# Kernel tuning notes

Measured on AMD Instinct MI355X. Metric: run time of the kernel, lower is better.

The kernel has to match this reference:

```python
import jax, jax.numpy as jnp
import numpy as np
import math

SIZE = 64
NLAND = 8
N_ITER = 6


def setup_inputs() -> dict:
    key = jax.random.key(0)
    k1, k2, k3 = jax.random.split(key, 3)
    B, T, C = 4, 4096, 1024
    return {
        "q": jax.random.normal(k1, (B, T, C), dtype=jnp.float32),
        "k": jax.random.normal(k2, (B, T, C), dtype=jnp.float32),
        "v": jax.random.normal(k3, (B, T, C), dtype=jnp.float32),
    }


def _iterative_pinv(mat, n_iter=N_ITER):
    # Newton-Schulz iteration for pseudo-inverse of [..., m, m] kernel.
    m = mat.shape[-1]
    I = jnp.eye(m, dtype=mat.dtype)
    K = mat
    # NOTE: torch.max over the whole tensor (global scalar), faithful to source.
    V = (1.0 / jnp.max(jnp.sum(K, axis=-2))) * jnp.swapaxes(K, -1, -2)
    for _ in range(n_iter):
        KV = jnp.matmul(K, V)
        V = jnp.matmul(0.25 * V, 13.0 * I - jnp.matmul(KV, 15.0 * I - jnp.matmul(KV, 7.0 * I - KV)))
    return V


def reference(q, k, v):
    B, T, C = q.shape
    H = C // SIZE
    scale = 1.0 / math.sqrt(SIZE)
    # Faithful reshape (not transpose) as in the source module.
    qh = q.reshape(B, H, T, SIZE)
    kh = k.reshape(B, H, T, SIZE)
    vh = v.reshape(B, H, T, SIZE)
    # T % NLAND == 0 branch: landmark = segment mean over T//NLAND tokens.
    q_l = qh.reshape(B, H, NLAND, T // NLAND, SIZE).mean(axis=-2)  # [B,H,m,d]
    k_l = kh.reshape(B, H, NLAND, T // NLAND, SIZE).mean(axis=-2)
    kernel_1 = jax.nn.softmax(jnp.einsum('bhtd,bhmd->bhtm', qh, k_l) * scale, axis=-1)  # [B,H,T,m]
    kernel_2 = jax.nn.softmax(jnp.einsum('bhmd,bhnd->bhmn', q_l, k_l) * scale, axis=-1)  # [B,H,m,m]
    kernel_3 = jax.nn.softmax(jnp.einsum('bhmd,bhtd->bhmt', q_l, kh) * scale, axis=-1)  # [B,H,m,T]
    pinv = _iterative_pinv(kernel_2)  # [B,H,m,m]
    k3v = jnp.matmul(kernel_3, vh)    # [B,H,m,d]
    out = jnp.matmul(jnp.matmul(kernel_1, pinv), k3v)  # [B,H,T,d]
    return out.reshape(B, T, C)
```

## Files before the change

### kernel.cpp

```cpp
#include <hip/hip_runtime.h>
#include <math.h>

#define T_TOK 4096
#define DD 64
#define NHEADS 64
#define SEG 512
#define NCHUNK 32
#define CHUNK 128
#define TILE 32
#define SCALE 0.125f

#define QL_OFF   0
#define KL_OFF   32768
#define K2_OFF   65536
#define CS_OFF   69632
#define PINV_OFF 70144
#define LPQ_OFF  74240
#define KP_OFF   205312
#define PA_OFF   336384
#define PD_OFF   1384960
#define W2_OFF   1401344

__global__ __launch_bounds__(256) void qsum_kernel(
    const float* __restrict__ q, float* __restrict__ ws) {
  int tid = threadIdx.x;
  const float4* q4 = (const float4*)q + (size_t)blockIdx.x * 2048;
  float4 a = make_float4(0.f, 0.f, 0.f, 0.f);
#pragma unroll
  for (int it = 0; it < 8; ++it) {
    float4 x = q4[it * 256 + tid];
    a.x += x.x; a.y += x.y; a.z += x.z; a.w += x.w;
  }
  __shared__ float4 red[16][17];
  red[tid >> 4][tid & 15] = a;
  __syncthreads();
  if (tid < 16) {
    float4 s = make_float4(0.f, 0.f, 0.f, 0.f);
#pragma unroll
    for (int g = 0; g < 16; ++g) {
      float4 r = red[g][tid];
      s.x += r.x; s.y += r.y; s.z += r.z; s.w += r.w;
    }
    ((float4*)(ws + LPQ_OFF))[blockIdx.x * 16 + tid] = s;
  }
}

__global__ __launch_bounds__(512) void prepq_kernel(float* __restrict__ ws) {
  int hb = blockIdx.x, tid = threadIdx.x;
  int m = tid >> 6, d = tid & 63;
  float s = 0.f;
#pragma unroll
  for (int c2 = 0; c2 < 4; ++c2)
    s += ws[LPQ_OFF + (size_t)(hb * 32 + m * 4 + c2) * 64 + d];
  ws[QL_OFF + hb * 512 + tid] = s * (1.f / (float)SEG);
}

__global__ __launch_bounds__(256) void k3v_kernel(
    const float* __restrict__ k, const float* __restrict__ v,
    float* __restrict__ ws) {
  int hb = blockIdx.x >> 5, c = blockIdx.x & 31;
  int tid = threadIdx.x;
  int w = tid >> 6, lane = tid & 63;
  __shared__ float ql[8][68];
  __shared__ float kt[TILE][68];
  __shared__ float vt[TILE][68];
  __shared__ float pl[TILE][9];
  __shared__ float denp[4][8];

  if (tid < 128) {
    float4 x = ((const float4*)(ws + QL_OFF))[hb * 128 + tid];
    *(float4*)&ql[tid >> 4][(tid & 15) * 4] = x;
  }
  size_t base4 = ((size_t)hb * T_TOK + (size_t)c * CHUNK) * 16;
  float a0 = 0.f, a1 = 0.f, dden = 0.f, ksum = 0.f;

  for (int tile = 0; tile < 4; ++tile) {
    __syncthreads();
    const float4* k4 = (const float4*)k + base4 + tile * TILE * 16;
    const float4* v4 = (const float4*)v + base4 + tile * TILE * 16;
    {
      float4 x0 = k4[tid], x1 = k4[tid + 256];
      float4 y0 = v4[tid], y1 = v4[tid + 256];
      *(float4*)&kt[tid >> 4][(tid & 15) * 4] = x0;
      *(float4*)&kt[(tid + 256) >> 4][(tid & 15) * 4] = x1;
      *(float4*)&vt[tid >> 4][(tid & 15) * 4] = y0;
      *(float4*)&vt[(tid + 256) >> 4][(tid & 15) * 4] = y1;
    }
    __syncthreads();
    {
      int t = tid >> 3, m = tid & 7;
      const float4* kr = (const float4*)&kt[t][0];
      const float4* qr = (const float4*)&ql[m][0];
      float dot = 0.f;
#pragma unroll
      for (int d4 = 0; d4 < 16; ++d4) {
        float4 kk = kr[d4], qq = qr[d4];
        dot += kk.x * qq.x + kk.y * qq.y + kk.z * qq.z + kk.w * qq.w;
      }
      float p = __expf(dot * SCALE);
      pl[t][m] = p;
      float r = p;
      r += __shfl_xor(r, 8);
      r += __shfl_xor(r, 16);
      r += __shfl_xor(r, 32);
      if (lane < 8) denp[w][lane] = r;
    }
    __syncthreads();
    {
#pragma unroll
      for (int t = 0; t < TILE; ++t) {
        float vv = vt[t][lane];
        a0 += pl[t][w] * vv;
        a1 += pl[t][w + 4] * vv;
      }
      if (w == 0) {
#pragma unroll
        for (int t = 0; t < TILE; ++t) ksum += kt[t][lane];
      }
      if (tid < 8)
        dden += denp[0][tid] + denp[1][tid] + denp[2][tid] + denp[3][tid];
    }
  }
  ws[PA_OFF + (((size_t)hb * NCHUNK + c) * 8 + w) * 64 + lane] = a0;
  ws[PA_OFF + (((size_t)hb * NCHUNK + c) * 8 + w + 4) * 64 + lane] = a1;
  if (tid < 8) ws[PD_OFF + (hb * NCHUNK + c) * 8 + tid] = dden;
  if (tid < 64) ws[KP_OFF + (size_t)(hb * NCHUNK + c) * 64 + tid] = ksum;
}

__global__ __launch_bounds__(512) void prepk_kernel(float* __restrict__ ws) {
  int hb = blockIdx.x, tid = threadIdx.x;
  __shared__ float qls[8][68];
  __shared__ float kls[8][68];
  __shared__ float ee[8][9];
  int m = tid >> 6, d = tid & 63;
  float s = 0.f;
#pragma unroll
  for (int c2 = 0; c2 < 4; ++c2)
    s += ws[KP_OFF + (size_t)(hb * 32 + m * 4 + c2) * 64 + d];
  s *= (1.f / (float)SEG);
  kls[m][d] = s;
  ws[KL_OFF + hb * 512 + tid] = s;
  qls[m][d] = ws[QL_OFF + hb * 512 + tid];
  __syncthreads();
  if (tid < 64) {
    int i = tid >> 3, j = tid & 7;
    float dot = 0.f;
#pragma unroll
    for (int dd = 0; dd < 64; ++dd) dot += qls[i][dd] * kls[j][dd];
    ee[i][j] = __expf(dot * SCALE);
  }
  __syncthreads();
  if (tid < 64) {
    int i = tid >> 3, j = tid & 7;
    float ssum = 0.f;
#pragma unroll
    for (int jj = 0; jj < 8; ++jj) ssum += ee[i][jj];
    ws[K2_OFF + hb * 64 + tid] = ee[i][j] / ssum;
  }
  if (tid < 8) {
    float cs = 0.f;
    for (int ii = 0; ii < 8; ++ii) {
      float ssum = 0.f;
#pragma unroll
      for (int jj = 0; jj < 8; ++jj) ssum += ee[ii][jj];
      cs += ee[ii][tid] / ssum;
    }
    ws[CS_OFF + hb * 8 + tid] = cs;
  }
}

__global__ __launch_bounds__(64) void pinv_kernel(float* __restrict__ ws) {
  int hb = blockIdx.x;
  int tid = threadIdx.x;
  float mx = 0.f;
  for (int t = 0; t < 8; ++t) mx = fmaxf(mx, ws[CS_OFF + t * 64 + tid]);
  for (int off = 32; off; off >>= 1) mx = fmaxf(mx, __shfl_xor(mx, off));
  float inv = 1.f / mx;

  int i = tid >> 3, j = tid & 7;
  __shared__ float K[8][9], V[8][9], X[8][9], Y[8][9];
  K[i][j] = ws[K2_OFF + hb * 64 + tid];
  V[i][j] = ws[K2_OFF + hb * 64 + j * 8 + i] * inv;
  __syncthreads();
  for (int it = 0; it < 6; ++it) {
    float x = 0.f;
    for (int kk = 0; kk < 8; ++kk) x += K[i][kk] * V[kk][j];
    X[i][j] = x;
    __syncthreads();
    float bm = 0.f;
    for (int kk = 0; kk < 8; ++kk) bm += X[i][kk] * X[kk][j];
    bm = 7.f * x - bm;
    Y[i][j] = bm;
    __syncthreads();
    float dm = 0.f;
    for (int kk = 0; kk < 8; ++kk) dm += X[i][kk] * Y[kk][j];
    dm = 15.f * x - dm;
    __syncthreads();
    Y[i][j] = dm;
    __syncthreads();
    float vd = 0.f;
    for (int kk = 0; kk < 8; ++kk) vd += V[i][kk] * Y[kk][j];
    float vn = 0.25f * (13.f * V[i][j] - vd);
    __syncthreads();
    V[i][j] = vn;
    __syncthreads();
  }
  ws[PINV_OFF + hb * 64 + tid] = V[i][j];
}

__global__ __launch_bounds__(512) void redw2_kernel(float* __restrict__ ws) {
  int hb = blockIdx.x, tid = threadIdx.x;
  __shared__ float k3vs[8][68];
  __shared__ float pv[8][9];
  int m = tid >> 6, d = tid & 63;
  float s = 0.f, den = 0.f;
  for (int c = 0; c < NCHUNK; ++c) {
    s += ws[PA_OFF + (((size_t)hb * NCHUNK + c) * 8 + m) * 64 + d];
    den += ws[PD_OFF + (hb * NCHUNK + c) * 8 + m];
  }
  k3vs[m][d] = s / den;
  if (tid < 64) pv[tid >> 3][tid & 7] = ws[PINV_OFF + hb * 64 + tid];
  __syncthreads();
  float o = 0.f;
#pragma unroll
  for (int j = 0; j < 8; ++j) o += pv[m][j] * k3vs[j][d];
  ws[W2_OFF + hb * 512 + tid] = o;
}

__global__ __launch_bounds__(256) void out_kernel(
    const float* __restrict__ q, float* __restrict__ out,
    const float* __restrict__ ws) {
  int hb = blockIdx.x >> 6, tt = blockIdx.x & 63;
  int tid = threadIdx.x;
  __shared__ float qt[64][68];
  __shared__ float klh[8][68];
  __shared__ float w2s[8][68];
  __shared__ float pl[64][9];

  if (tid < 128) {
    float4 x = ((const float4*)(ws + KL_OFF))[hb * 128 + tid];
    *(float4*)&klh[tid >> 4][(tid & 15) * 4] = x;
    float4 y = ((const float4*)(ws + W2_OFF))[hb * 128 + tid];
    *(float4*)&w2s[tid >> 4][(tid & 15) * 4] = y;
  }
  size_t base4 = ((size_t)hb * T_TOK + (size_t)tt * 64) * 16;
  const float4* q4 = (const float4*)q + base4;
#pragma unroll
  for (int it = 0; it < 4; ++it) {
    int f4 = it * 256 + tid;
    float4 x = q4[f4];
    *(float4*)&qt[f4 >> 4][(f4 & 15) * 4] = x;
  }
  __syncthreads();
#pragma unroll
  for (int p = 0; p < 2; ++p) {
    int idx = p * 256 + tid;
    int t = idx >> 3, m = idx & 7;
    const float4* qr = (const float4*)&qt[t][0];
    const float4* kr = (const float4*)&klh[m][0];
    float dot = 0.f;
#pragma unroll
    for (int d4 = 0; d4 < 16; ++d4) {
      float4 a = qr[d4], b = kr[d4];
      dot += a.x * b.x + a.y * b.y + a.z * b.z + a.w * b.w;
    }
    pl[t][m] = __expf(dot * SCALE);
  }
  __syncthreads();
  float4* o4 = (float4*)out + base4;
#pragma unroll
  for (int i = 0; i < 4; ++i) {
    int t = i * 16 + (tid >> 4);
    int qd = tid & 15;
    float p0 = pl[t][0], p1 = pl[t][1], p2 = pl[t][2], p3 = pl[t][3];
    float p4 = pl[t][4], p5 = pl[t][5], p6 = pl[t][6], p7 = pl[t][7];
    float inv = 1.f / (p0 + p1 + p2 + p3 + p4 + p5 + p6 + p7);
    float4 acc = make_float4(0.f, 0.f, 0.f, 0.f);
    float pm[8] = {p0, p1, p2, p3, p4, p5, p6, p7};
#pragma unroll
    for (int m2 = 0; m2 < 8; ++m2) {
      float w = pm[m2] * inv;
      float4 wv = *(const float4*)&w2s[m2][qd * 4];
      acc.x += w * wv.x; acc.y += w * wv.y; acc.z += w * wv.z; acc.w += w * wv.w;
    }
    o4[i * 256 + tid] = acc;
  }
}

extern "C" void kernel_launch(void* const* d_in, const int* in_sizes, int n_in,
                              void* d_out, int out_size, void* d_ws, size_t ws_size,
                              hipStream_t stream) {
  const float* q = (const float*)d_in[0];
  const float* k = (const float*)d_in[1];
  const float* v = (const float*)d_in[2];
  float* out = (float*)d_out;
  float* ws = (float*)d_ws;

  qsum_kernel<<<2048, 256, 0, stream>>>(q, ws);
  prepq_kernel<<<NHEADS, 512, 0, stream>>>(ws);
  k3v_kernel<<<NHEADS * NCHUNK, 256, 0, stream>>>(k, v, ws);
  prepk_kernel<<<NHEADS, 512, 0, stream>>>(ws);
  pinv_kernel<<<NHEADS, 64, 0, stream>>>(ws);
  redw2_kernel<<<NHEADS, 512, 0, stream>>>(ws);
  out_kernel<<<NHEADS * 64, 256, 0, stream>>>(q, out, ws);
}
```

Baseline: 93.05 us.

## Split k3v into separate K-pass and V-pass kernels; fuse pinv into W2 kernel

Replaces the combined K/V chunk kernel with a K pass that computes landmark-query softmax numerators via wave shuffles and stores per-token probabilities to workspace, and a separate V pass that reads those probabilities and accumulates P·V in registers. It also merges the Newton-Schulz pseudo-inverse into the reduction/W2 kernel, removing one launch. The intent is to cut LDS traffic and barriers in the streaming passes. The cost is an extra workspace round trip for the probability matrix and an additional full-grid launch.

```diff
diff --git a/kernel.cpp b/kernel.cpp
--- a/kernel.cpp
+++ b/kernel.cpp
@@ -7,19 +7,18 @@
 #define SEG 512
 #define NCHUNK 32
 #define CHUNK 128
-#define TILE 32
 #define SCALE 0.125f
 
 #define QL_OFF   0
 #define KL_OFF   32768
 #define K2_OFF   65536
 #define CS_OFF   69632
-#define PINV_OFF 70144
 #define LPQ_OFF  74240
 #define KP_OFF   205312
-#define PA_OFF   336384
-#define PD_OFF   1384960
-#define W2_OFF   1401344
+#define PA_OFF   74240
+#define PD_OFF   1122816
+#define W2_OFF   1139200
+#define P_OFF    1171968
 
 __global__ __launch_bounds__(256) void qsum_kernel(
     const float* __restrict__ q, float* __restrict__ ws) {
@@ -55,76 +54,73 @@
   ws[QL_OFF + hb * 512 + tid] = s * (1.f / (float)SEG);
 }
 
-__global__ __launch_bounds__(256) void k3v_kernel(
-    const float* __restrict__ k, const float* __restrict__ v,
-    float* __restrict__ ws) {
+__global__ __launch_bounds__(256) void ppass_kernel(
+    const float* __restrict__ k, float* __restrict__ ws) {
+  int tid = threadIdx.x;
+  int w = tid >> 6, lane = tid & 63, q4i = lane & 15, g = lane >> 4;
   int hb = blockIdx.x >> 5, c = blockIdx.x & 31;
-  int tid = threadIdx.x;
-  int w = tid >> 6, lane = tid & 63;
-  __shared__ float ql[8][68];
-  __shared__ float kt[TILE][68];
-  __shared__ float vt[TILE][68];
-  __shared__ float pl[TILE][9];
-  __shared__ float denp[4][8];
-
-  if (tid < 128) {
-    float4 x = ((const float4*)(ws + QL_OFF))[hb * 128 + tid];
-    *(float4*)&ql[tid >> 4][(tid & 15) * 4] = x;
-  }
-  size_t base4 = ((size_t)hb * T_TOK + (size_t)c * CHUNK) * 16;
-  float a0 = 0.f, a1 = 0.f, dden = 0.f, ksum = 0.f;
-
-  for (int tile = 0; tile < 4; ++tile) {
-    __syncthreads();
-    const float4* k4 = (const float4*)k + base4 + tile * TILE * 16;
-    const float4* v4 = (const float4*)v + base4 + tile * TILE * 16;
-    {
-      float4 x0 = k4[tid], x1 = k4[tid + 256];
-      float4 y0 = v4[tid], y1 = v4[tid + 256];
-      *(float4*)&kt[tid >> 4][(tid & 15) * 4] = x0;
-      *(float4*)&kt[(tid + 256) >> 4][(tid & 15) * 4] = x1;
-      *(float4*)&vt[tid >> 4][(tid & 15) * 4] = y0;
-      *(float4*)&vt[(tid + 256) >> 4][(tid & 15) * 4] = y1;
-    }
-    __syncthreads();
-    {
-      int t = tid >> 3, m = tid & 7;
-      const float4* kr = (const float4*)&kt[t][0];
-      const float4* qr = (const float4*)&ql[m][0];
-      float dot = 0.f;
-#pragma unroll
-      for (int d4 = 0; d4 < 16; ++d4) {
-        float4 kk = kr[d4], qq = qr[d4];
-        dot += kk.x * qq.x + kk.y * qq.y + kk.z * qq.z + kk.w * qq.w;
-      }
-      float p = __expf(dot * SCALE);
-      pl[t][m] = p;
-      float r = p;
-      r += __shfl_xor(r, 8);
-      r += __shfl_xor(r, 16);
-      r += __shfl_xor(r, 32);
-      if (lane < 8) denp[w][lane] = r;
-    }
-    __syncthreads();
-    {
-#pragma unroll
-      for (int t = 0; t < TILE; ++t) {
-        float vv = vt[t][lane];
-        a0 += pl[t][w] * vv;
-        a1 += pl[t][w + 4] * vv;
-      }
-      if (w == 0) {
-#pragma unroll
-        for (int t = 0; t < TILE; ++t) ksum += kt[t][lane];
-      }
-      if (tid < 8)
-        dden += denp[0][tid] + denp[1][tid] + denp[2][tid] + denp[3][tid];
-    }
-  }
-  ws[PA_OFF + (((size_t)hb * NCHUNK + c) * 8 + w) * 64 + lane] = a0;
-  ws[PA_OFF + (((size_t)hb * NCHUNK + c) * 8 + w + 4) * 64 + lane] = a1;
-  if (tid < 8) ws[PD_OFF + (hb * NCHUNK + c) * 8 + tid] = dden;
-  if (tid < 64) ws[KP_OFF + (size_t)(hb * NCHUNK + c) * 64 + tid] = ksum;
+
+  float4 qlf[8];
+#pragma unroll
+  for (int m = 0; m < 8; ++m)
+    qlf[m] = ((const float4*)(ws + QL_OFF))[hb * 128 + m * 16 + q4i];
+
+  size_t tokbase = (size_t)hb * T_TOK + (size_t)c * CHUNK + (size_t)w * 32;
+  const float4* k4 = (const float4*)k + tokbase * 16;
+
+  float4 ksum = make_float4(0.f, 0.f, 0.f, 0.f);
+  float den[8];
+#pragma unroll
+  for (int m = 0; m < 8; ++m) den[m] = 0.f;
+
+#pragma unroll 2
+  for (int it = 0; it < 8; ++it) {
+    float4 kk = k4[it * 64 + lane];
+    ksum.x += kk.x; ksum.y += kk.y; ksum.z += kk.z; ksum.w += kk.w;
+    float p[8];
+#pragma unroll
+    for (int m = 0; m < 8; ++m) {
+      float dp = kk.x * qlf[m].x + kk.y * qlf[m].y + kk.z * qlf[m].z + kk.w * qlf[m].w;
+      dp += __shfl_xor(dp, 1, 64);
+      dp += __shfl_xor(dp, 2, 64);
+      dp += __shfl_xor(dp, 4, 64);
+      dp += __shfl_xor(dp, 8, 64);
+      p[m] = __expf(dp * SCALE);
+      den[m] += p[m];
+    }
+    float pw = q4i == 1 ? p[1] : q4i == 2 ? p[2] : q4i == 3 ? p[3] :
+               q4i == 4 ? p[4] : q4i == 5 ? p[5] : q4i == 6 ? p[6] :
+               q4i == 7 ? p[7] : p[0];
+    if (q4i < 8)
+      ws[P_OFF + (tokbase + it * 4 + g) * 8 + q4i] = pw;
+  }
+#pragma unroll
+  for (int m = 0; m < 8; ++m) {
+    den[m] += __shfl_xor(den[m], 16, 64);
+    den[m] += __shfl_xor(den[m], 32, 64);
+  }
+#pragma unroll
+  for (int s = 16; s <= 32; s <<= 1) {
+    ksum.x += __shfl_xor(ksum.x, s, 64); ksum.y += __shfl_xor(ksum.y, s, 64);
+    ksum.z += __shfl_xor(ksum.z, s, 64); ksum.w += __shfl_xor(ksum.w, s, 64);
+  }
+  __shared__ float4 ksums[4][16];
+  __shared__ float dens[4][8];
+  if (lane < 16) ksums[w][lane] = ksum;
+  float dw = q4i == 1 ? den[1] : q4i == 2 ? den[2] : q4i == 3 ? den[3] :
+             q4i == 4 ? den[4] : q4i == 5 ? den[5] : q4i == 6 ? den[6] :
+             q4i == 7 ? den[7] : den[0];
+  if (lane < 8) dens[w][lane] = dw;
+  __syncthreads();
+  if (tid < 16) {
+    float4 a = ksums[0][tid], b = ksums[1][tid], cc = ksums[2][tid], dd = ksums[3][tid];
+    float4 s = make_float4(a.x + b.x + cc.x + dd.x, a.y + b.y + cc.y + dd.y,
+                           a.z + b.z + cc.z + dd.z, a.w + b.w + cc.w + dd.w);
+    ((float4*)(ws + KP_OFF))[(size_t)(hb * 32 + c) * 16 + tid] = s;
+  }
+  if (tid < 8)
+    ws[PD_OFF + (hb * 32 + c) * 8 + tid] =
+        dens[0][tid] + dens[1][tid] + dens[2][tid] + dens[3][tid];
 }
 
 __global__ __launch_bounds__(512) void prepk_kernel(float* __restrict__ ws) {
@@ -169,49 +165,68 @@
   }
 }
 
-__global__ __launch_bounds__(64) void pinv_kernel(float* __restrict__ ws) {
-  int hb = blockIdx.x;
+__global__ __launch_bounds__(256) void vpass_kernel(
+    const float* __restrict__ v, float* __restrict__ ws) {
   int tid = threadIdx.x;
-  float mx = 0.f;
-  for (int t = 0; t < 8; ++t) mx = fmaxf(mx, ws[CS_OFF + t * 64 + tid]);
-  for (int off = 32; off; off >>= 1) mx = fmaxf(mx, __shfl_xor(mx, off));
-  float inv = 1.f / mx;
-
-  int i = tid >> 3, j = tid & 7;
-  __shared__ float K[8][9], V[8][9], X[8][9], Y[8][9];
-  K[i][j] = ws[K2_OFF + hb * 64 + tid];
-  V[i][j] = ws[K2_OFF + hb * 64 + j * 8 + i] * inv;
-  __syncthreads();
-  for (int it = 0; it < 6; ++it) {
-    float x = 0.f;
-    for (int kk = 0; kk < 8; ++kk) x += K[i][kk] * V[kk][j];
-    X[i][j] = x;
-    __syncthreads();
-    float bm = 0.f;
-    for (int kk = 0; kk < 8; ++kk) bm += X[i][kk] * X[kk][j];
-    bm = 7.f * x - bm;
-    Y[i][j] = bm;
-    __syncthreads();
-    float dm = 0.f;
-    for (int kk = 0; kk < 8; ++kk) dm += X[i][kk] * Y[kk][j];
-    dm = 15.f * x - dm;
-    __syncthreads();
-    Y[i][j] = dm;
-    __syncthreads();
-    float vd = 0.f;
-    for (int kk = 0; kk < 8; ++kk) vd += V[i][kk] * Y[kk][j];
-    float vn = 0.25f * (13.f * V[i][j] - vd);
-    __syncthreads();
-    V[i][j] = vn;
-    __syncthreads();
-  }
-  ws[PINV_OFF + hb * 64 + tid] = V[i][j];
-}
-
-__global__ __launch_bounds__(512) void redw2_kernel(float* __restrict__ ws) {
+  int w = tid >> 6, lane = tid & 63, g = lane >> 4;
+  int hb = blockIdx.x >> 5, c = blockIdx.x & 31;
+
+  size_t tokbase = (size_t)hb * T_TOK + (size_t)c * CHUNK + (size_t)w * 32;
+  float4 pf = ((const float4*)(ws + P_OFF))[tokbase * 2 + lane];
+  __shared__ float plds[4][260];
+  *(float4*)&plds[w][lane * 4] = pf;
+  __syncthreads();
+
+  const float4* v4 = (const float4*)v + tokbase * 16;
+  float4 acc[8];
+#pragma unroll
+  for (int m = 0; m < 8; ++m) acc[m] = make_float4(0.f, 0.f, 0.f, 0.f);
+
+#pragma unroll 2
+  for (int it = 0; it < 8; ++it) {
+    float4 vv = v4[it * 64 + lane];
+    int t = it * 4 + g;
+    float4 pa = *(const float4*)&plds[w][t * 8];
+    float4 pb = *(const float4*)&plds[w][t * 8 + 4];
+    acc[0].x += pa.x * vv.x; acc[0].y += pa.x * vv.y; acc[0].z += pa.x * vv.z; acc[0].w += pa.x * vv.w;
+    acc[1].x += pa.y * vv.x; acc[1].y += pa.y * vv.y; acc[1].z += pa.y * vv.z; acc[1].w += pa.y * vv.w;
+    acc[2].x += pa.z * vv.x; acc[2].y += pa.z * vv.y; acc[2].z += pa.z * vv.z; acc[2].w += pa.z * vv.w;
+    acc[3].x += pa.w * vv.x; acc[3].y += pa.w * vv.y; acc[3].z += pa.w * vv.z; acc[3].w += pa.w * vv.w;
+    acc[4].x += pb.x * vv.x; acc[4].y += pb.x * vv.y; acc[4].z += pb.x * vv.z; acc[4].w += pb.x * vv.w;
+    acc[5].x += pb.y * vv.x; acc[5].y += pb.y * vv.y; acc[5].z += pb.y * vv.z; acc[5].w += pb.y * vv.w;
+    acc[6].x += pb.z * vv.x; acc[6].y += pb.z * vv.y; acc[6].z += pb.z * vv.z; acc[6].w += pb.z * vv.w;
+    acc[7].x += pb.w * vv.x; acc[7].y += pb.w * vv.y; acc[7].z += pb.w * vv.z; acc[7].w += pb.w * vv.w;
+  }
+#pragma unroll
+  for (int m = 0; m < 8; ++m) {
+#pragma unroll
+    for (int s = 16; s <= 32; s <<= 1) {
+      acc[m].x += __shfl_xor(acc[m].x, s, 64);
+      acc[m].y += __shfl_xor(acc[m].y, s, 64);
+      acc[m].z += __shfl_xor(acc[m].z, s, 64);
+      acc[m].w += __shfl_xor(acc[m].w, s, 64);
+    }
+  }
+  __shared__ float4 accs[4][8][17];
+  if (lane < 16) {
+#pragma unroll
+    for (int m = 0; m < 8; ++m) accs[w][m][lane] = acc[m];
+  }
+  __syncthreads();
+  if (tid < 128) {
+    int m = tid >> 4, i = tid & 15;
+    float4 a = accs[0][m][i], b = accs[1][m][i], cc = accs[2][m][i], dd = accs[3][m][i];
+    float4 s = make_float4(a.x + b.x + cc.x + dd.x, a.y + b.y + cc.y + dd.y,
+                           a.z + b.z + cc.z + dd.z, a.w + b.w + cc.w + dd.w);
+    ((float4*)(ws + PA_OFF))[((size_t)(hb * 32 + c) * 8 + m) * 16 + i] = s;
+  }
+}
+
+__global__ __launch_bounds__(512) void pinvw2_kernel(float* __restrict__ ws) {
   int hb = blockIdx.x, tid = threadIdx.x;
   __shared__ float k3vs[8][68];
-  __shared__ float pv[8][9];
+  __shared__ float K[8][9], V[8][9], X[8][9], Y[8][9];
+  __shared__ float smax;
   int m = tid >> 6, d = tid & 63;
   float s = 0.f, den = 0.f;
   for (int c = 0; c < NCHUNK; ++c) {
@@ -219,20 +234,63 @@
     den += ws[PD_OFF + (hb * NCHUNK + c) * 8 + m];
   }
   k3vs[m][d] = s / den;
-  if (tid < 64) pv[tid >> 3][tid & 7] = ws[PINV_OFF + hb * 64 + tid];
-  __syncthreads();
+  if (tid < 64) {
+    float mx = 0.f;
+    for (int t = 0; t < 8; ++t) mx = fmaxf(mx, ws[CS_OFF + t * 64 + tid]);
+    for (int off = 32; off; off >>= 1) mx = fmaxf(mx, __shfl_xor(mx, off, 64));
+    if (tid == 0) smax = mx;
+  }
+  int i = (tid >> 3) & 7, j = tid & 7;
+  if (tid < 64) {
+    K[i][j] = ws[K2_OFF + hb * 64 + tid];
+  }
+  __syncthreads();
+  if (tid < 64) V[i][j] = K[j][i] * (1.f / smax);
+  __syncthreads();
+  for (int it = 0; it < 6; ++it) {
+    float x = 0.f;
+    if (tid < 64) {
+      for (int kk = 0; kk < 8; ++kk) x += K[i][kk] * V[kk][j];
+      X[i][j] = x;
+    }
+    __syncthreads();
+    float bm = 0.f;
+    if (tid < 64) {
+      for (int kk = 0; kk < 8; ++kk) bm += X[i][kk] * X[kk][j];
+      bm = 7.f * x - bm;
+      Y[i][j] = bm;
+    }
+    __syncthreads();
+    float dm = 0.f;
+    if (tid < 64) {
+      for (int kk = 0; kk < 8; ++kk) dm += X[i][kk] * Y[kk][j];
+      dm = 15.f * x - dm;
+    }
+    __syncthreads();
+    if (tid < 64) Y[i][j] = dm;
+    __syncthreads();
+    float vd = 0.f;
+    if (tid < 64) {
+      for (int kk = 0; kk < 8; ++kk) vd += V[i][kk] * Y[kk][j];
+      vd = 0.25f * (13.f * V[i][j] - vd);
+    }
+    __syncthreads();
+    if (tid < 64) V[i][j] = vd;
+    __syncthreads();
+  }
   float o = 0.f;
 #pragma unroll
-  for (int j = 0; j < 8; ++j) o += pv[m][j] * k3vs[j][d];
+  for (int jj = 0; jj < 8; ++jj) o += V[m][jj] * k3vs[jj][d];
   ws[W2_OFF + hb * 512 + tid] = o;
 }
 
+#define PADT 68
 __global__ __launch_bounds__(256) void out_kernel(
     const float* __restrict__ q, float* __restrict__ out,
     const float* __restrict__ ws) {
   int hb = blockIdx.x >> 6, tt = blockIdx.x & 63;
   int tid = threadIdx.x;
-  __shared__ float qt[64][68];
+  __shared__ float qt[64][PADT];
   __shared__ float klh[8][68];
   __shared__ float w2s[8][68];
   __shared__ float pl[64][9];
@@ -298,9 +356,9 @@
 
   qsum_kernel<<<2048, 256, 0, stream>>>(q, ws);
   prepq_kernel<<<NHEADS, 512, 0, stream>>>(ws);
-  k3v_kernel<<<NHEADS * NCHUNK, 256, 0, stream>>>(k, v, ws);
+  ppass_kernel<<<NHEADS * NCHUNK, 256, 0, stream>>>(k, ws);
   prepk_kernel<<<NHEADS, 512, 0, stream>>>(ws);
-  pinv_kernel<<<NHEADS, 64, 0, stream>>>(ws);
-  redw2_kernel<<<NHEADS, 512, 0, stream>>>(ws);
+  vpass_kernel<<<NHEADS * NCHUNK, 256, 0, stream>>>(v, ws);
+  pinvw2_kernel<<<NHEADS, 512, 0, stream>>>(ws);
   out_kernel<<<NHEADS * 64, 256, 0, stream>>>(q, out, ws);
 }
```

Result: slower. 106.7 us (+14.7%).
